# Optimization experiments

Measured on AMD Instinct MI355X. Metric: run time of the kernel, lower is better.

The kernel has to match this reference:

```python
import jax, jax.numpy as jnp
import numpy as np

D_MODEL = 1024
NUM_HEADS = 16
MAX_SEQ_LEN = 2048
THETA = 10000.0
D_K = D_MODEL // NUM_HEADS


def setup_inputs() -> dict:
    key = jax.random.key(0)
    ks = jax.random.split(key, 5)
    x = jax.random.normal(ks[0], (2, 2048, D_MODEL), dtype=jnp.float32)
    token_positions = jnp.arange(2048, dtype=jnp.int32)
    s = 1.0 / np.sqrt(D_MODEL)
    w_q = jax.random.normal(ks[1], (D_MODEL, D_MODEL), dtype=jnp.float32) * s
    w_k = jax.random.normal(ks[2], (D_MODEL, D_MODEL), dtype=jnp.float32) * s
    w_v = jax.random.normal(ks[3], (D_MODEL, D_MODEL), dtype=jnp.float32) * s
    w_o = jax.random.normal(ks[4], (D_MODEL, D_MODEL), dtype=jnp.float32) * s
    return {"x": x, "token_positions": token_positions,
            "w_q": w_q, "w_k": w_k, "w_v": w_v, "w_o": w_o}


def _rope_tables():
    inv_freq = 1.0 / (THETA ** (jnp.arange(0, D_K, 2, dtype=jnp.float32) / D_K))
    angles = jnp.arange(MAX_SEQ_LEN, dtype=jnp.float32)[:, None] * inv_freq[None, :]
    return jnp.cos(angles), jnp.sin(angles)  # [max_seq_len, d_k//2]


def _apply_rope(x, cos, sin):
    # x: [..., s, d_k]; interleaved-pair rotation, cos/sin: [s, d_k//2]
    x0 = x[..., 0::2]
    x1 = x[..., 1::2]
    y0 = x0 * cos - x1 * sin
    y1 = x0 * sin + x1 * cos
    return jnp.stack((y0, y1), axis=-1).reshape(x.shape)


def reference(x, token_positions, w_q, w_k, w_v, w_o):
    b, s, _ = x.shape
    h, dk = NUM_HEADS, D_K
    # torch Linear: y = x @ W^T
    q = (x @ w_q.T).reshape(b, s, h, dk).transpose(0, 2, 1, 3)  # [b,h,s,dk]
    k = (x @ w_k.T).reshape(b, s, h, dk).transpose(0, 2, 1, 3)
    v = (x @ w_v.T).reshape(b, s, h, dk).transpose(0, 2, 1, 3)
    cos_c, sin_c = _rope_tables()
    cos = cos_c[token_positions]  # [s, dk//2]
    sin = sin_c[token_positions]
    q = _apply_rope(q, cos, sin)
    k = _apply_rope(k, cos, sin)
    scores = jnp.einsum('bhqd,bhkd->bhqk', q, k) / jnp.sqrt(jnp.float32(dk))
    causal = jnp.tril(jnp.ones((s, s), dtype=bool))
    scores = jnp.where(causal, scores, -jnp.inf)
    attn = jax.nn.softmax(scores, axis=-1)
    out = jnp.einsum('bhqk,bhkd->bhqd', attn, v)
    out = out.transpose(0, 2, 1, 3).reshape(b, s, h * dk)
    return out @ w_o.T
```

## Files before the change

### kernel.cpp

```cpp
#include <hip/hip_runtime.h>
#include <cstdint>
#include <cstddef>

#define DEV static __device__ __forceinline__

typedef __attribute__((ext_vector_type(8))) short bf16x8;
typedef __attribute__((ext_vector_type(4))) float f32x4;

DEV uint16_t f2bf(float f) {
  uint32_t u = __builtin_bit_cast(uint32_t, f);
  u += 0x7FFFu + ((u >> 16) & 1u);
  return (uint16_t)(u >> 16);
}

DEV uint16_t f2bf_trunc(float f) {
  return (uint16_t)(__builtin_bit_cast(uint32_t, f) >> 16);
}

DEV float fexp2(float x) { return __builtin_amdgcn_exp2f(x); }

template <int CTRL>
DEV float dppf(float v) {
  return __builtin_bit_cast(
      float, __builtin_amdgcn_update_dpp(0, __builtin_bit_cast(int, v), CTRL, 0xF, 0xF, true));
}
DEV float rowmax16(float v) {
  v = fmaxf(v, dppf<0xB1>(v));
  v = fmaxf(v, dppf<0x4E>(v));
  v = fmaxf(v, dppf<0x124>(v));
  v = fmaxf(v, dppf<0x128>(v));
  return v;
}
DEV float rowsum16(float v) {
  v += dppf<0xB1>(v);
  v += dppf<0x4E>(v);
  v += dppf<0x124>(v);
  v += dppf<0x128>(v);
  return v;
}

DEV void load_lds16(const void* g, void* l) {
  auto gp = reinterpret_cast<const uint32_t __attribute__((address_space(1)))*>(
      reinterpret_cast<uintptr_t>(g));
  auto lp = reinterpret_cast<uint32_t __attribute__((address_space(3)))*>(
      reinterpret_cast<uintptr_t>(l));
  __builtin_amdgcn_global_load_lds(gp, lp, 16, 0, 0);
}

__global__ __launch_bounds__(256) void cvt_all(const float* __restrict__ x,
                                               const float* __restrict__ wq,
                                               const float* __restrict__ wk,
                                               const float* __restrict__ wv,
                                               const float* __restrict__ wo,
                                               const int* __restrict__ tokpos,
                                               uint16_t* __restrict__ dst,
                                               float2* __restrict__ rtab) {
  int bx = blockIdx.x;
  if (bx >= 8192) {
    int idx = (bx - 8192) * 256 + threadIdx.x;
    int s = idx >> 5, f = idx & 31;
    float invf = __expf(-0.28782314f * (float)f);
    float pos = (float)tokpos[s];
    float sn, cs;
    __sincosf(pos * invf, &sn, &cs);
    rtab[idx] = make_float2(cs, sn);
    return;
  }
  int gi = bx * 1024 + threadIdx.x * 4;
  const float* s;
  int li;
  if (gi < 4194304) {
    s = x; li = gi;
  } else {
    int j = gi - 4194304;
    int r = j >> 20;
    li = j & 1048575;
    s = (r == 0) ? wq : (r == 1) ? wk : (r == 2) ? wv : wo;
  }
  float4 v = *reinterpret_cast<const float4*>(s + li);
  ushort4 o;
  o.x = f2bf(v.x); o.y = f2bf(v.y); o.z = f2bf(v.z); o.w = f2bf(v.w);
  *reinterpret_cast<ushort4*>(dst + gi) = o;
}

__global__ __launch_bounds__(256) void gemm_qkv(const uint16_t* __restrict__ A,
                                                const uint16_t* __restrict__ Wqkv,
                                                uint16_t* __restrict__ QK,
                                                uint16_t* __restrict__ VTb,
                                                const float2* __restrict__ rtab) {
  __shared__ union {
    struct { uint16_t a[128 * 64]; uint16_t b[128 * 64]; } st;
    uint16_t t[128 * 128];
  } sm;

  const int tid = threadIdx.x;
  const int lane = tid & 63, w = tid >> 6;
  const int q = lane >> 4, l16 = lane & 15;
  const int wm = w & 1, wn = w >> 1;
  const int bm = blockIdx.y, bn = blockIdx.x;
  const int wsel = bn >> 3;

  const f32x4 z4 = {0.f, 0.f, 0.f, 0.f};
  f32x4 acc[4][4];
#pragma unroll
  for (int i = 0; i < 4; ++i)
#pragma unroll
    for (int j = 0; j < 4; ++j) acc[i][j] = z4;

  const int srow = tid >> 3, sslot = tid & 7;
  const uint16_t* Ab = A + (size_t)bm * 128 * 1024;
  const uint16_t* Bb = Wqkv + (size_t)bn * 128 * 1024;

  for (int k0 = 0; k0 < 1024; k0 += 64) {
    __syncthreads();
#pragma unroll
    for (int is = 0; is < 4; ++is) {
      int row = is * 32 + srow;
      int gch = sslot ^ (row & 7);
      char* la = (char*)sm.st.a + (is * 32 + w * 8) * 128;
      char* lb = (char*)sm.st.b + (is * 32 + w * 8) * 128;
      load_lds16(Ab + (size_t)row * 1024 + k0 + gch * 8, la);
      load_lds16(Bb + (size_t)row * 1024 + k0 + gch * 8, lb);
    }
    __syncthreads();
#pragma unroll
    for (int ks = 0; ks < 2; ++ks) {
      bf16x8 af[4], bfr[4];
#pragma unroll
      for (int i = 0; i < 4; ++i) {
        int ra = wm * 64 + i * 16 + l16;
        af[i] = *reinterpret_cast<const bf16x8*>(sm.st.a + ra * 64 +
                                                 (((ks * 4 + q) ^ (ra & 7)) * 8));
        int rb = wn * 64 + i * 16 + l16;
        bfr[i] = *reinterpret_cast<const bf16x8*>(sm.st.b + rb * 64 +
                                                  (((ks * 4 + q) ^ (rb & 7)) * 8));
      }
#pragma unroll
      for (int i = 0; i < 4; ++i)
#pragma unroll
        for (int j = 0; j < 4; ++j)
          acc[i][j] =
              __builtin_amdgcn_mfma_f32_16x16x32_bf16(af[i], bfr[j], acc[i][j], 0, 0, 0);
    }
  }

  if (wsel < 2) {
    uint16_t* O = QK + (size_t)wsel * 4194304;
    const float scq = (wsel == 0) ? 0.18033688f : 1.0f;
#pragma unroll
    for (int j = 0; j < 4; ++j) {
      int gn = bn * 128 + wn * 64 + j * 16 + l16;
      int cn = gn & 1023;
      int f = (gn & 63) >> 1;
      float sgn = (lane & 1) ? 1.f : -1.f;
#pragma unroll
      for (int i = 0; i < 4; ++i) {
#pragma unroll
        for (int r = 0; r < 4; ++r) {
          int gm = bm * 128 + wm * 64 + i * 16 + q * 4 + r;
          float2 cssn = rtab[(gm & 2047) * 32 + f];
          float v = acc[i][j][r];
          float o = dppf<0xB1>(v);
          O[(size_t)gm * 1024 + cn] = f2bf((v * cssn.x + sgn * o * cssn.y) * scq);
        }
      }
    }
  } else {
    const int bnv = bn & 7;
    __syncthreads();
#pragma unroll
    for (int i = 0; i < 4; ++i)
#pragma unroll
      for (int j = 0; j < 4; ++j)
#pragma unroll
        for (int r = 0; r < 4; ++r) {
          int mL = wm * 64 + i * 16 + q * 4 + r;
          int nL = wn * 64 + j * 16 + l16;
          int ch = (mL >> 3) ^ (nL & 15);
          sm.t[nL * 128 + ch * 8 + (mL & 7)] = f2bf(acc[i][j][r]);
        }
    __syncthreads();
    const int b = (bm * 128) >> 11;
    const int sblk = (bm * 128) & 2047;
#pragma unroll
    for (int it = 0; it < 8; ++it) {
      int nL = it * 16 + (tid >> 4);
      int mch = tid & 15;
      int slot = mch ^ (nL & 15);
      bf16x8 vv = *reinterpret_cast<const bf16x8*>(sm.t + nL * 128 + slot * 8);
      int gn = bnv * 128 + nL;
      int h = gn >> 6, d = gn & 63;
      *reinterpret_cast<bf16x8*>(VTb + ((size_t)((b * 16 + h) * 64 + d)) * 2048 + sblk +
                                 mch * 8) = vv;
    }
  }
}

__global__ __launch_bounds__(256) void gemm_out(const uint16_t* __restrict__ A,
                                                const uint16_t* __restrict__ Bw,
                                                float* __restrict__ O) {
  __shared__ uint16_t sa[128 * 64];
  __shared__ uint16_t sb[64 * 64];

  const int tid = threadIdx.x;
  const int lane = tid & 63, w = tid >> 6;
  const int q = lane >> 4, l16 = lane & 15;
  const int bm = blockIdx.y, bn = blockIdx.x;

  const f32x4 z4 = {0.f, 0.f, 0.f, 0.f};
  f32x4 acc[2][4];
#pragma unroll
  for (int i = 0; i < 2; ++i)
#pragma unroll
    for (int j = 0; j < 4; ++j) acc[i][j] = z4;

  const int srow = tid >> 3, sslot = tid & 7;
  const uint16_t* Ab = A + (size_t)bm * 128 * 1024;
  const uint16_t* Bb = Bw + (size_t)bn * 64 * 1024;

  for (int k0 = 0; k0 < 1024; k0 += 64) {
    __syncthreads();
#pragma unroll
    for (int is = 0; is < 4; ++is) {
      int row = is * 32 + srow;
      int gch = sslot ^ (row & 7);
      load_lds16(Ab + (size_t)row * 1024 + k0 + gch * 8,
                 (char*)sa + (is * 32 + w * 8) * 128);
    }
#pragma unroll
    for (int is = 0; is < 2; ++is) {
      int row = is * 32 + srow;
      int gch = sslot ^ (row & 7);
      load_lds16(Bb + (size_t)row * 1024 + k0 + gch * 8,
                 (char*)sb + (is * 32 + w * 8) * 128);
    }
    __syncthreads();
#pragma unroll
    for (int ks = 0; ks < 2; ++ks) {
      bf16x8 af[2], bfr[4];
#pragma unroll
      for (int i = 0; i < 2; ++i) {
        int ra = w * 32 + i * 16 + l16;
        af[i] = *reinterpret_cast<const bf16x8*>(sa + ra * 64 +
                                                 (((ks * 4 + q) ^ (ra & 7)) * 8));
      }
#pragma unroll
      for (int j = 0; j < 4; ++j) {
        int rb = j * 16 + l16;
        bfr[j] = *reinterpret_cast<const bf16x8*>(sb + rb * 64 +
                                                  (((ks * 4 + q) ^ (rb & 7)) * 8));
      }
#pragma unroll
      for (int i = 0; i < 2; ++i)
#pragma unroll
        for (int j = 0; j < 4; ++j)
          acc[i][j] =
              __builtin_amdgcn_mfma_f32_16x16x32_bf16(af[i], bfr[j], acc[i][j], 0, 0, 0);
    }
  }

#pragma unroll
  for (int i = 0; i < 2; ++i)
#pragma unroll
    for (int r = 0; r < 4; ++r) {
      int gm = bm * 128 + w * 32 + i * 16 + q * 4 + r;
#pragma unroll
      for (int j = 0; j < 4; ++j) {
        int gn = bn * 64 + j * 16 + l16;
        O[(size_t)gm * 1024 + gn] = acc[i][j][r];
      }
    }
}

__global__ __launch_bounds__(512) void flash_attn(const uint16_t* __restrict__ Q,
                                                  const uint16_t* __restrict__ K,
                                                  const uint16_t* __restrict__ VT,
                                                  uint16_t* __restrict__ AO) {
  __shared__ uint16_t ksm[2][128 * 64];
  __shared__ uint16_t vsm[2][64 * 128];
  __shared__ uint16_t psm[8][16 * 128];

  const int tid = threadIdx.x;
  const int lane = tid & 63, w = tid >> 6;
  const int q = lane >> 4, l16 = lane & 15;
  const int p = blockIdx.x;
  const int bh = blockIdx.y;
  const int b = bh >> 4, h = bh & 15;

  const size_t baseBS = (size_t)b * 2048 * 1024 + h * 64;
  const size_t baseVT = (size_t)bh * 64 * 2048;
  uint16_t* pw = psm[w];
  const f32x4 z4 = {0.f, 0.f, 0.f, 0.f};

  auto stage = [&](int buf, int kt) {
#pragma unroll
    for (int is = 0; is < 2; ++is) {
      int row = is * 64 + (tid >> 3);
      int gch = (tid & 7) ^ (row & 7);
      load_lds16(K + baseBS + (size_t)(kt * 128 + row) * 1024 + gch * 8,
                 (char*)ksm[buf] + (is * 64 + w * 8) * 128);
    }
#pragma unroll
    for (int is = 0; is < 2; ++is) {
      int row = is * 32 + (tid >> 4);
      int gch = (tid & 15) ^ (row & 15);
      load_lds16(VT + baseVT + (size_t)row * 2048 + kt * 128 + gch * 8,
                 (char*)vsm[buf] + (is * 32 + w * 4) * 256);
    }
  };

  for (int t = 0; t < 2; ++t) {
    const int qt = t ? (15 - p) : p;
    const int r0 = qt * 128 + w * 16;
    const int nkt = qt + 1;

    bf16x8 qf[2];
#pragma unroll
    for (int ks = 0; ks < 2; ++ks)
      qf[ks] = *reinterpret_cast<const bf16x8*>(
          Q + baseBS + (size_t)(r0 + l16) * 1024 + ks * 32 + q * 8);

    f32x4 oa[4];
#pragma unroll
    for (int di = 0; di < 4; ++di) oa[di] = z4;
    float m2[4], li[4];
#pragma unroll
    for (int r = 0; r < 4; ++r) { m2[r] = -1e30f; li[r] = 0.f; }

    __syncthreads();
    stage(0, 0);

    for (int kt = 0; kt < nkt; ++kt) {
      const int cur = kt & 1;
      __syncthreads();
      if (kt + 1 < nkt) stage(cur ^ 1, kt + 1);

      f32x4 sc[8];
#pragma unroll
      for (int nj = 0; nj < 8; ++nj) sc[nj] = z4;
#pragma unroll
      for (int ks = 0; ks < 2; ++ks) {
        bf16x8 kf[8];
#pragma unroll
        for (int nj = 0; nj < 8; ++nj) {
          int rk = nj * 16 + l16;
          kf[nj] = *reinterpret_cast<const bf16x8*>(ksm[cur] + rk * 64 +
                                                    (((ks * 4 + q) ^ (rk & 7)) * 8));
        }
#pragma unroll
        for (int nj = 0; nj < 8; ++nj)
          sc[nj] =
              __builtin_amdgcn_mfma_f32_16x16x32_bf16(qf[ks], kf[nj], sc[nj], 0, 0, 0);
      }

      if (kt == nkt - 1) {
#pragma unroll
        for (int nj = 0; nj < 8; ++nj)
#pragma unroll
          for (int r = 0; r < 4; ++r) {
            int col = kt * 128 + nj * 16 + l16;
            int row = r0 + q * 4 + r;
            if (col > row) sc[nj][r] = -1e30f;
          }
      }

      float alpha[4];
#pragma unroll
      for (int r = 0; r < 4; ++r) {
        float v = fmaxf(
            fmaxf(fmaxf(sc[0][r], sc[1][r]), fmaxf(sc[2][r], sc[3][r])),
            fmaxf(fmaxf(sc[4][r], sc[5][r]), fmaxf(sc[6][r], sc[7][r])));
        v = rowmax16(v);
        float mn = fmaxf(m2[r], v);
        alpha[r] = fexp2(m2[r] - mn);
        m2[r] = mn;
        li[r] *= alpha[r];
      }

#pragma unroll
      for (int nj = 0; nj < 8; ++nj)
#pragma unroll
        for (int r = 0; r < 4; ++r) {
          float pv = fexp2(sc[nj][r] - m2[r]);
          li[r] += pv;
          int pr = q * 4 + r;
          int pc = nj * 16 + l16;
          pw[pr * 128 + (((pc >> 3) ^ (pr & 15)) * 8) + (pc & 7)] = f2bf_trunc(pv);
        }

#pragma unroll
      for (int di = 0; di < 4; ++di)
#pragma unroll
        for (int r = 0; r < 4; ++r) oa[di][r] *= alpha[r];

#pragma unroll
      for (int ks = 0; ks < 4; ++ks) {
        bf16x8 pf;
        {
          int pr = l16;
          pf = *reinterpret_cast<const bf16x8*>(pw + pr * 128 +
                                                (((ks * 4 + q) ^ (pr & 15)) * 8));
        }
        bf16x8 vf[4];
#pragma unroll
        for (int di = 0; di < 4; ++di) {
          int vr = di * 16 + l16;
          vf[di] = *reinterpret_cast<const bf16x8*>(vsm[cur] + vr * 128 +
                                                    (((ks * 4 + q) ^ (vr & 15)) * 8));
        }
#pragma unroll
        for (int di = 0; di < 4; ++di)
          oa[di] =
              __builtin_amdgcn_mfma_f32_16x16x32_bf16(pf, vf[di], oa[di], 0, 0, 0);
      }
    }

#pragma unroll
    for (int r = 0; r < 4; ++r) {
      float inv = 1.f / rowsum16(li[r]);
      int gm = r0 + q * 4 + r;
#pragma unroll
      for (int di = 0; di < 4; ++di)
        AO[baseBS + (size_t)gm * 1024 + di * 16 + l16] = f2bf(oa[di][r] * inv);
    }
  }
}

extern "C" void kernel_launch(void* const* d_in, const int* in_sizes, int n_in,
                              void* d_out, int out_size, void* d_ws, size_t ws_size,
                              hipStream_t stream) {
  (void)in_sizes; (void)n_in; (void)out_size; (void)ws_size;
  const float* x = (const float*)d_in[0];
  const int* tokpos = (const int*)d_in[1];
  const float* wq = (const float*)d_in[2];
  const float* wk = (const float*)d_in[3];
  const float* wv = (const float*)d_in[4];
  const float* wo = (const float*)d_in[5];
  float* out = (float*)d_out;

  uint16_t* ws = (uint16_t*)d_ws;
  uint16_t* xb = ws;
  uint16_t* wqb = xb + 4194304;
  uint16_t* wob = wqb + 3145728;
  uint16_t* Qb = wob + 1048576;
  uint16_t* VTb = Qb + 8388608;
  uint16_t* AOb = VTb + 4194304;
  float2* rtab = (float2*)AOb;

  cvt_all<<<8448, 256, 0, stream>>>(x, wq, wk, wv, wo, tokpos, xb, rtab);

  gemm_qkv<<<dim3(24, 32), 256, 0, stream>>>(xb, wqb, Qb, VTb, rtab);

  flash_attn<<<dim3(8, 32), 512, 0, stream>>>(Qb, Qb + 4194304, VTb, AOb);

  gemm_out<<<dim3(16, 32), 256, 0, stream>>>(AOb, wob, out);
}
```

Baseline: 185.3 us.

## Double-buffer LDS tiles in QKV and output projection GEMMs

Both GEMM kernels now keep two LDS buffers for the A and B tiles. While the current tile is consumed by MFMAs, the next K-slice's global-to-LDS loads are issued into the other buffer, leaving one barrier per iteration instead of two. The aim is to hide global load latency behind matrix compute. In exchange, LDS usage per block doubles, which may reduce the number of resident blocks per CU.

```diff
diff --git a/kernel.cpp b/kernel.cpp
--- a/kernel.cpp
+++ b/kernel.cpp
@@ -89,7 +89,7 @@
                                                 uint16_t* __restrict__ VTb,
                                                 const float2* __restrict__ rtab) {
   __shared__ union {
-    struct { uint16_t a[128 * 64]; uint16_t b[128 * 64]; } st;
+    struct { uint16_t a[2][128 * 64]; uint16_t b[2][128 * 64]; } st;
     uint16_t t[128 * 128];
   } sm;
 
@@ -111,28 +111,33 @@
   const uint16_t* Ab = A + (size_t)bm * 128 * 1024;
   const uint16_t* Bb = Wqkv + (size_t)bn * 128 * 1024;
 
-  for (int k0 = 0; k0 < 1024; k0 += 64) {
-    __syncthreads();
+  auto stage = [&](int buf, int k0) {
 #pragma unroll
     for (int is = 0; is < 4; ++is) {
       int row = is * 32 + srow;
       int gch = sslot ^ (row & 7);
-      char* la = (char*)sm.st.a + (is * 32 + w * 8) * 128;
-      char* lb = (char*)sm.st.b + (is * 32 + w * 8) * 128;
+      char* la = (char*)sm.st.a[buf] + (is * 32 + w * 8) * 128;
+      char* lb = (char*)sm.st.b[buf] + (is * 32 + w * 8) * 128;
       load_lds16(Ab + (size_t)row * 1024 + k0 + gch * 8, la);
       load_lds16(Bb + (size_t)row * 1024 + k0 + gch * 8, lb);
     }
+  };
+
+  stage(0, 0);
+  for (int t = 0; t < 16; ++t) {
+    const int cur = t & 1;
     __syncthreads();
+    if (t + 1 < 16) stage(cur ^ 1, (t + 1) * 64);
 #pragma unroll
     for (int ks = 0; ks < 2; ++ks) {
       bf16x8 af[4], bfr[4];
 #pragma unroll
       for (int i = 0; i < 4; ++i) {
         int ra = wm * 64 + i * 16 + l16;
-        af[i] = *reinterpret_cast<const bf16x8*>(sm.st.a + ra * 64 +
+        af[i] = *reinterpret_cast<const bf16x8*>(sm.st.a[cur] + ra * 64 +
                                                  (((ks * 4 + q) ^ (ra & 7)) * 8));
         int rb = wn * 64 + i * 16 + l16;
-        bfr[i] = *reinterpret_cast<const bf16x8*>(sm.st.b + rb * 64 +
+        bfr[i] = *reinterpret_cast<const bf16x8*>(sm.st.b[cur] + rb * 64 +
                                                   (((ks * 4 + q) ^ (rb & 7)) * 8));
       }
 #pragma unroll
@@ -199,8 +204,8 @@
 __global__ __launch_bounds__(256) void gemm_out(const uint16_t* __restrict__ A,
                                                 const uint16_t* __restrict__ Bw,
                                                 float* __restrict__ O) {
-  __shared__ uint16_t sa[128 * 64];
-  __shared__ uint16_t sb[64 * 64];
+  __shared__ uint16_t sa[2][128 * 64];
+  __shared__ uint16_t sb[2][64 * 64];
 
   const int tid = threadIdx.x;
   const int lane = tid & 63, w = tid >> 6;
@@ -218,36 +223,41 @@
   const uint16_t* Ab = A + (size_t)bm * 128 * 1024;
   const uint16_t* Bb = Bw + (size_t)bn * 64 * 1024;
 
-  for (int k0 = 0; k0 < 1024; k0 += 64) {
-    __syncthreads();
+  auto stage = [&](int buf, int k0) {
 #pragma unroll
     for (int is = 0; is < 4; ++is) {
       int row = is * 32 + srow;
       int gch = sslot ^ (row & 7);
       load_lds16(Ab + (size_t)row * 1024 + k0 + gch * 8,
-                 (char*)sa + (is * 32 + w * 8) * 128);
+                 (char*)sa[buf] + (is * 32 + w * 8) * 128);
     }
 #pragma unroll
     for (int is = 0; is < 2; ++is) {
       int row = is * 32 + srow;
       int gch = sslot ^ (row & 7);
       load_lds16(Bb + (size_t)row * 1024 + k0 + gch * 8,
-                 (char*)sb + (is * 32 + w * 8) * 128);
-    }
+                 (char*)sb[buf] + (is * 32 + w * 8) * 128);
+    }
+  };
+
+  stage(0, 0);
+  for (int t = 0; t < 16; ++t) {
+    const int cur = t & 1;
     __syncthreads();
+    if (t + 1 < 16) stage(cur ^ 1, (t + 1) * 64);
 #pragma unroll
     for (int ks = 0; ks < 2; ++ks) {
       bf16x8 af[2], bfr[4];
 #pragma unroll
       for (int i = 0; i < 2; ++i) {
         int ra = w * 32 + i * 16 + l16;
-        af[i] = *reinterpret_cast<const bf16x8*>(sa + ra * 64 +
+        af[i] = *reinterpret_cast<const bf16x8*>(sa[cur] + ra * 64 +
                                                  (((ks * 4 + q) ^ (ra & 7)) * 8));
       }
 #pragma unroll
       for (int j = 0; j < 4; ++j) {
         int rb = j * 16 + l16;
-        bfr[j] = *reinterpret_cast<const bf16x8*>(sb + rb * 64 +
+        bfr[j] = *reinterpret_cast<const bf16x8*>(sb[cur] + rb * 64 +
                                                   (((ks * 4 + q) ^ (rb & 7)) * 8));
       }
 #pragma unroll
```

Measured after the change: 182.2 us. Within noise of the previous version (-1.7%).
